# Performance work log

Hardware: AMD Instinct MI355X
Metric: run time of the kernel (lower is better)

Reference implementation:

```python
import jax, jax.numpy as jnp
import numpy as np

# --- constants from init_kwargs ---
ANCHORS = np.array([1.3221, 1.73145, 3.19275, 4.00944, 5.05587,
                    8.09892, 9.47112, 4.84053, 11.2364, 10.0071], np.float32).reshape(5, 2)
NA = 5           # num_anchors
NC = 1           # num_classes (per meta input)
CS = 20          # meta classes (target.size(1))
MAX_BOXES = 50
COORD_SCALE = 1.0
NOOBJ_SCALE = 1.0
OBJ_SCALE = 5.0
CLASS_SCALE = 1.0
SIL_THRESH = 0.6
N_META = 20      # enews buckets


def _iou(cx1, cy1, w1, h1, cx2, cy2, w2, h2):
    # center-format IoU, matching bbox_ious(..., x1y1x2y2=False)
    mx = jnp.minimum(cx1 - 0.5 * w1, cx2 - 0.5 * w2)
    Mx = jnp.maximum(cx1 + 0.5 * w1, cx2 + 0.5 * w2)
    my = jnp.minimum(cy1 - 0.5 * h1, cy2 - 0.5 * h2)
    My = jnp.maximum(cy1 + 0.5 * h1, cy2 + 0.5 * h2)
    cw = w1 + w2 - (Mx - mx)
    ch = h1 + h2 - (My - my)
    inter = jnp.where((cw > 0) & (ch > 0), cw * ch, 0.0)
    return inter / (w1 * h1 + w2 * h2 - inter)


def setup_inputs() -> dict:
    key = jax.random.key(0)
    k1, k2, k3, k4 = jax.random.split(key, 4)
    output = jax.random.normal(k1, (320, 30, 26, 26), dtype=jnp.float32)
    target = jax.random.uniform(k2, (16, 20, 250), dtype=jnp.float32)
    dynamic_weights = jax.random.normal(k3, (1, 64, 1024), dtype=jnp.float32)
    target_cls_ids = jax.random.randint(k4, (64,), 0, 20, dtype=jnp.int32)
    return {"output": output, "target": target,
            "dynamic_weights": dynamic_weights, "target_cls_ids": target_cls_ids}


def reference(output, target, dynamic_weights, target_cls_ids):
    target = jax.lax.stop_gradient(target)  # torch uses target.data
    dw = dynamic_weights[0]                 # (n_dw, D)

    nB, ch, nH, nW = output.shape
    bs = nB // CS
    K = NA * nH * nW
    out5 = output.reshape(nB, NA, 5 + NC, nH, nW)
    x = jax.nn.sigmoid(out5[:, :, 0])
    y = jax.nn.sigmoid(out5[:, :, 1])
    w = out5[:, :, 2]
    h = out5[:, :, 3]
    conf = jax.nn.sigmoid(out5[:, :, 4])
    # meta classification logits: softmax across the cs meta inputs
    cls_logits = out5[:, :, 5].reshape(bs, CS, K)  # nC == 1

    aw = jnp.asarray(ANCHORS[:, 0])
    ah = jnp.asarray(ANCHORS[:, 1])
    grid_x = jnp.arange(nW, dtype=jnp.float32)
    grid_y = jnp.arange(nH, dtype=jnp.float32)

    # decoded pred boxes (torch builds them from .data -> detached)
    px = jax.lax.stop_gradient(x) + grid_x[None, None, None, :]
    py = jax.lax.stop_gradient(y) + grid_y[None, None, :, None]
    pw = jnp.exp(jax.lax.stop_gradient(w)) * aw[None, :, None, None]
    ph = jnp.exp(jax.lax.stop_gradient(h)) * ah[None, :, None, None]

    # ---- build_targets (vectorized) ----
    g = target.reshape(nB, MAX_BOXES, 5)
    valid = g[:, :, 1] != 0
    gxs = g[:, :, 1] * nW
    gys = g[:, :, 2] * nH
    gws = g[:, :, 3] * nW
    ghs = g[:, :, 4] * nH

    pb = lambda t: t.reshape(nB, K, 1)
    ious = _iou(pb(px), pb(py), pb(pw), pb(ph),
                gxs[:, None, :], gys[:, None, :], gws[:, None, :], ghs[:, None, :])  # (nB,K,50)
    cur_ious = jnp.max(jnp.where(valid[:, None, :], ious, 0.0), axis=-1)
    conf_mask = jnp.where(cur_ious > SIL_THRESH, 0.0, NOOBJ_SCALE).reshape(nB, NA, nH, nW)

    # seen < 12800 branch (self.seen = 0)
    shape4 = (nB, NA, nH, nW)
    coord_mask = jnp.ones(shape4, jnp.float32)
    tx = jnp.full(shape4, 0.5, jnp.float32)
    ty = jnp.full(shape4, 0.5, jnp.float32)
    tw = jnp.zeros(shape4, jnp.float32)
    th = jnp.zeros(shape4, jnp.float32)
    tconf = jnp.zeros(shape4, jnp.float32)
    cls_mask = jnp.zeros(shape4, jnp.float32)

    # best anchor per gt by wh-IoU (anchor_step == 2)
    inter_a = jnp.minimum(gws[..., None], aw) * jnp.minimum(ghs[..., None], ah)
    iou_a = inter_a / (gws[..., None] * ghs[..., None] + aw * ah - inter_a)
    best_n = jnp.argmax(iou_a, axis=-1)  # (nB,50)

    gi = jnp.clip(gxs.astype(jnp.int32), 0, nW - 1)
    gj = jnp.clip(gys.astype(jnp.int32), 0, nH - 1)
    b_idx = jnp.broadcast_to(jnp.arange(nB)[:, None], (nB, MAX_BOXES))
    fidx = ((b_idx * NA + best_n) * nH + gj) * nW + gi
    fidx = jnp.where(valid, fidx, nB * NA * nH * nW).reshape(-1)  # OOB -> dropped

    def scat(base, vals):
        return base.reshape(-1).at[fidx].set(vals.reshape(-1), mode='drop').reshape(shape4)

    pbx = px[b_idx, best_n, gj, gi]
    pby = py[b_idx, best_n, gj, gi]
    pbw = pw[b_idx, best_n, gj, gi]
    pbh = ph[b_idx, best_n, gj, gi]
    iou_gt = _iou(gxs, gys, gws, ghs, pbx, pby, pbw, pbh)

    ones = jnp.ones_like(gxs)
    coord_mask = scat(coord_mask, ones)
    cls_mask = scat(cls_mask, ones)
    conf_mask = scat(conf_mask, jnp.full_like(gxs, OBJ_SCALE))
    tx = scat(tx, gxs - gi.astype(jnp.float32))
    ty = scat(ty, gys - gj.astype(jnp.float32))
    tw = scat(tw, jnp.log(gws / aw[best_n]))
    th = scat(th, jnp.log(ghs / ah[best_n]))
    tconf = scat(tconf, iou_gt)

    # ---- region losses ----
    loss_x = COORD_SCALE * 0.5 * jnp.sum(coord_mask * (x - tx) ** 2)
    loss_y = COORD_SCALE * 0.5 * jnp.sum(coord_mask * (y - ty) ** 2)
    loss_w = COORD_SCALE * 0.5 * jnp.sum(coord_mask * (w - tw) ** 2)
    loss_h = COORD_SCALE * 0.5 * jnp.sum(coord_mask * (h - th) ** 2)
    loss_conf = 0.5 * jnp.sum(conf_mask * (conf - tconf) ** 2)

    logp = jax.nn.log_softmax(jnp.transpose(cls_logits, (0, 2, 1)), axis=-1)  # (bs,K,CS)
    mask_bc = cls_mask.reshape(bs, CS, K)
    loss_cls = CLASS_SCALE * (-jnp.sum(mask_bc * jnp.transpose(logp, (0, 2, 1))))

    # ---- max-margin term over dynamic reweighting vectors ----
    cnt = jax.ops.segment_sum(jnp.ones(dw.shape[0], jnp.float32), target_cls_ids, N_META)
    sums = jax.ops.segment_sum(dw, target_cls_ids, N_META)
    enews = sums / jnp.maximum(cnt, 1.0)[:, None]
    present = cnt > 0
    same = jnp.sum((dw - enews[target_cls_ids]) ** 2)
    d = jnp.sum((enews[:, None, :] - enews[None, :, :]) ** 2, axis=-1)
    vp = present[:, None] & present[None, :] & (~jnp.eye(N_META, dtype=bool))
    dmin = jnp.min(jnp.where(vp, d, jnp.inf), axis=1)
    different = jnp.sum(jnp.where(jnp.any(vp, axis=1), dmin, 0.0))

    return loss_x + loss_y + loss_w + loss_h + loss_conf + loss_cls + same - different
```

## Files before the change

### kernel.cpp

```cpp
#include <hip/hip_runtime.h>
#include <math.h>

#define NB 320
#define NAC 5
#define NH 26
#define NW 26
#define CHW 676
#define KTOT 3380
#define BSTRIDE 20280
#define MAXB 50
#define CS 20
#define NMETA 20
#define DWROWS 64
#define DWDIM 1024
#define NPAIR (NMETA * NMETA)
#define NCBLK 4
#define NPARTR (NB * NCBLK)
#define NMETAY ((NSAMEPAIR + NCBLK - 1) / NCBLK)
#define NSAMEPAIR (NMETA + NPAIR)
#define NPART (NPARTR + NMETA)

__constant__ float c_aw[5] = {1.3221f, 3.19275f, 5.05587f, 9.47112f, 11.2364f};
__constant__ float c_ah[5] = {1.73145f, 4.00944f, 8.09892f, 4.84053f, 10.0071f};

__device__ __forceinline__ float rl_f(float v, int l) {
    return __int_as_float(__builtin_amdgcn_readlane(__float_as_int(v), l));
}

__global__ __launch_bounds__(256) void fused_k(const float* __restrict__ out,
                                               const float* __restrict__ target,
                                               const float* __restrict__ dw,
                                               const int* __restrict__ ids,
                                               float* __restrict__ part,
                                               float* __restrict__ dmat) {
    __shared__ float sred[4];
    int tid = threadIdx.x;
    int lane = tid & 63;
    int wid = tid >> 6;
    int b = blockIdx.y;

    if (b >= NB) {
        int p = (b - NB) * NCBLK + blockIdx.x;
        float s = 0.0f;
        if (p < NMETA) {
            int c = p;
            float acc[4] = {0, 0, 0, 0}, ssq[4] = {0, 0, 0, 0};
            int cnt = 0;
            for (int r = 0; r < DWROWS; r++) {
                int idr = ids[r];
                if (idr == c) {
                    cnt++;
#pragma unroll
                    for (int k = 0; k < 4; k++) {
                        float v = dw[r * DWDIM + tid + k * 256];
                        acc[k] += v; ssq[k] += v * v;
                    }
                }
            }
            if (cnt > 0) {
                float inv = 1.0f / (float)cnt;
#pragma unroll
                for (int k = 0; k < 4; k++) {
                    float e = acc[k] * inv;
                    s += ssq[k] - (float)cnt * e * e;
                }
            }
        } else {
            int pp = p - NMETA;
            int pi = pp / NMETA, pj = pp - pi * NMETA;
            if (pi != pj) {
                float ai[4] = {0, 0, 0, 0}, aj[4] = {0, 0, 0, 0};
                int ci = 0, cj = 0;
                for (int r = 0; r < DWROWS; r++) {
                    int idr = ids[r];
                    if (idr == pi) {
                        ci++;
#pragma unroll
                        for (int k = 0; k < 4; k++) ai[k] += dw[r * DWDIM + tid + k * 256];
                    } else if (idr == pj) {
                        cj++;
#pragma unroll
                        for (int k = 0; k < 4; k++) aj[k] += dw[r * DWDIM + tid + k * 256];
                    }
                }
                float ii = 1.0f / fmaxf((float)ci, 1.0f);
                float ij = 1.0f / fmaxf((float)cj, 1.0f);
#pragma unroll
                for (int k = 0; k < 4; k++) {
                    float df = ai[k] * ii - aj[k] * ij;
                    s += df * df;
                }
            }
        }
#pragma unroll
        for (int o = 32; o > 0; o >>= 1) s += __shfl_down(s, o, 64);
        if (lane == 0) sred[wid] = s;
        __syncthreads();
        if (tid == 0) {
            float tot = sred[0] + sred[1] + sred[2] + sred[3];
            if (p < NMETA) part[NPARTR + p] = tot;
            else dmat[p - NMETA] = tot;
        }
        return;
    }

    float blox = 1e30f, bhix = -1e30f, bloy = 1e30f, bhiy = -1e30f, bta = 0.0f;
    float gx = 0.0f, gy = 0.0f, gw = 0.0f, gh = 0.0f;
    bool bvalid;
    {
        int t = (lane < MAXB) ? lane : 0;
        const float* g = target + b * (MAXB * 5) + t * 5;
        float g1 = g[1];
        gx = g1 * (float)NW;
        gy = g[2] * (float)NH;
        gw = g[3] * (float)NW;
        gh = g[4] * (float)NH;
        bvalid = (g1 != 0.0f) && (lane < MAXB);
        if (bvalid) {
            blox = gx - 0.5f * gw; bhix = gx + 0.5f * gw;
            bloy = gy - 0.5f * gh; bhiy = gy + 0.5f * gh;
            bta = 0.375f * gw * gh;
        }
    }

    bool isbox = (blockIdx.x == NCBLK - 1) && (wid == 2);
    float contrib = 0.0f;

    if (!isbox) {
        int k0 = blockIdx.x * 1024 + tid * 4;
        if (k0 < KTOT) {
            int a = k0 / CHW;
            int rem0 = k0 - a * CHW;
            const float* base = out + (size_t)b * BSTRIDE + a * 6 * CHW + rem0;
            float4 R0 = *(const float4*)(base + 0 * CHW);
            float4 R1 = *(const float4*)(base + 1 * CHW);
            float4 R2 = *(const float4*)(base + 2 * CHW);
            float4 R3 = *(const float4*)(base + 3 * CHW);
            float4 R4 = *(const float4*)(base + 4 * CHW);
            float RX[4] = {R0.x, R0.y, R0.z, R0.w};
            float RY[4] = {R1.x, R1.y, R1.z, R1.w};
            float RW[4] = {R2.x, R2.y, R2.z, R2.w};
            float RH[4] = {R3.x, R3.y, R3.z, R3.w};
            float RC[4] = {R4.x, R4.y, R4.z, R4.w};
            float X[4], Y[4], CF[4];
            float PLOX[4], PHIX[4], PLOY[4], PHIY[4], THR[4], SM[4];
            float aw = c_aw[a], ah = c_ah[a];
#pragma unroll
            for (int c = 0; c < 4; c++) {
                int rem = rem0 + c;
                int i = rem / NW;
                int j = rem - i * NW;
                float x = 1.0f / (1.0f + __expf(-RX[c]));
                float y = 1.0f / (1.0f + __expf(-RY[c]));
                float conf = 1.0f / (1.0f + __expf(-RC[c]));
                float pw = __expf(RW[c]) * aw;
                float ph = __expf(RH[c]) * ah;
                float px = x + (float)j;
                float py = y + (float)i;
                PLOX[c] = px - 0.5f * pw; PHIX[c] = px + 0.5f * pw;
                PLOY[c] = py - 0.5f * ph; PHIY[c] = py + 0.5f * ph;
                THR[c] = 0.375f * (pw * ph);
                SM[c] = -1e30f;
                X[c] = x; Y[c] = y; CF[c] = conf;
            }
#pragma unroll 10
            for (int tb = 0; tb < MAXB; tb++) {
                float thix = rl_f(bhix, tb), tlox = rl_f(blox, tb);
                float thiy = rl_f(bhiy, tb), tloy = rl_f(bloy, tb);
                float ta   = rl_f(bta, tb);
#pragma unroll
                for (int c = 0; c < 4; c++) {
                    float ix = fminf(PHIX[c], thix) - fmaxf(PLOX[c], tlox);
                    float iy = fminf(PHIY[c], thiy) - fmaxf(PLOY[c], tloy);
                    float ixc = fmaxf(ix, 0.0f), iyc = fmaxf(iy, 0.0f);
                    SM[c] = fmaxf(SM[c], __builtin_fmaf(ixc, iyc, -ta));
                }
            }
#pragma unroll
            for (int c = 0; c < 4; c++) {
                float dx = X[c] - 0.5f, dy = Y[c] - 0.5f;
                contrib += 0.5f * (dx * dx + dy * dy + RW[c] * RW[c] + RH[c] * RH[c]);
                if (!(SM[c] > THR[c])) contrib += 0.5f * CF[c] * CF[c];
            }
        }
    } else {
        int t = lane;
        int fidx = -1 - t;
        int bn = 0, gi = 0, gj = 0;
        if (bvalid) {
            float area = gw * gh;
            float best = -1.0f;
#pragma unroll
            for (int n = 0; n < 5; n++) {
                float inter = fminf(gw, c_aw[n]) * fminf(gh, c_ah[n]);
                float iou = inter / (area + c_aw[n] * c_ah[n] - inter);
                if (iou > best) { best = iou; bn = n; }
            }
            gi = min(max((int)gx, 0), NW - 1);
            gj = min(max((int)gy, 0), NH - 1);
            fidx = (bn * NH + gj) * NW + gi;
        }
        bool winner = bvalid;
        for (int t2 = 1; t2 < MAXB; t2++) {
            int f2 = __builtin_amdgcn_readlane(fidx, t2);
            winner = winner && ((t2 <= t) || (f2 != fidx));
        }
        if (winner) {
            int rem = gj * NW + gi;
            const float* cell = out + (size_t)b * BSTRIDE + bn * 6 * CHW + rem;
            float rx = cell[0 * CHW];
            float ry = cell[1 * CHW];
            float w  = cell[2 * CHW];
            float h  = cell[3 * CHW];
            float rc = cell[4 * CHW];
            float x = 1.0f / (1.0f + __expf(-rx));
            float y = 1.0f / (1.0f + __expf(-ry));
            float conf = 1.0f / (1.0f + __expf(-rc));
            float aw = c_aw[bn], ah = c_ah[bn];
            float pw = __expf(w) * aw;
            float ph = __expf(h) * ah;
            float px = x + (float)gi;
            float py = y + (float)gj;
            float plox = px - 0.5f * pw, phix = px + 0.5f * pw;
            float ploy = py - 0.5f * ph, phiy = py + 0.5f * ph;
            float parea = pw * ph;
            float thr = 0.375f * parea;
            float smax = -1e30f;
            for (int tb = 0; tb < MAXB; tb++) {
                float thix = rl_f(bhix, tb), tlox = rl_f(blox, tb);
                float thiy = rl_f(bhiy, tb), tloy = rl_f(bloy, tb);
                float ta   = rl_f(bta, tb);
                float ix = fminf(phix, thix) - fmaxf(plox, tlox);
                float iy = fminf(phiy, thiy) - fmaxf(ploy, tloy);
                smax = fmaxf(smax, __builtin_fmaf(fmaxf(ix, 0.0f), fmaxf(iy, 0.0f), -ta));
            }
            bool silent = smax > thr;
            float dx0 = x - 0.5f, dy0 = y - 0.5f;
            float basel = 0.5f * (dx0 * dx0 + dy0 * dy0 + w * w + h * h);
            if (!silent) basel += 0.5f * conf * conf;
            float ix = fminf(phix, bhix) - fmaxf(plox, blox);
            float iy = fminf(phiy, bhiy) - fmaxf(ploy, bloy);
            float inter = fmaxf(ix, 0.0f) * fmaxf(iy, 0.0f);
            float iou = inter / (parea + gw * gh - inter);
            float txv = gx - (float)gi, tyv = gy - (float)gj;
            float twv = __logf(gw / aw), thv = __logf(gh / ah);
            float dx = x - txv, dy = y - tyv;
            float dwv = w - twv, dhv = h - thv;
            float dc = conf - iou;
            float ovr = 0.5f * (dx * dx + dy * dy + dwv * dwv + dhv * dhv) + 2.5f * dc * dc;
            int bs = b / CS, cs = b - bs * CS;
            const float* cl = out + (size_t)(bs * CS) * BSTRIDE + (bn * 6 + 5) * CHW + rem;
            float v[CS];
            float m = -1e30f;
#pragma unroll
            for (int c2 = 0; c2 < CS; c2++) { v[c2] = cl[(size_t)c2 * BSTRIDE]; m = fmaxf(m, v[c2]); }
            float s = 0.0f, own = 0.0f;
#pragma unroll
            for (int c2 = 0; c2 < CS; c2++) {
                s += __expf(v[c2] - m);
                if (c2 == cs) own = v[c2];
            }
            contrib = ovr - basel + (m + __logf(s)) - own;
        }
    }

#pragma unroll
    for (int o = 32; o > 0; o >>= 1) contrib += __shfl_down(contrib, o, 64);
    if (lane == 0) sred[wid] = contrib;
    __syncthreads();
    if (tid == 0) part[b * NCBLK + blockIdx.x] = sred[0] + sred[1] + sred[2] + sred[3];
}

__global__ __launch_bounds__(256) void finish_k(const int* __restrict__ ids,
                                                const float* __restrict__ part,
                                                const float* __restrict__ dmat,
                                                float* __restrict__ loss) {
    __shared__ float sred[4];
    __shared__ int scnt[NMETA];
    __shared__ float sdd;
    int tid = threadIdx.x;
    int lane = tid & 63, wid = tid >> 6;

    if (tid < NMETA) {
        int c = 0;
        for (int r = 0; r < DWROWS; r++) c += (ids[r] == tid) ? 1 : 0;
        scnt[tid] = c;
    }
    __syncthreads();
    float dd = 0.0f;
    if (tid < NMETA && scnt[tid] > 0) {
        float dmin = INFINITY;
        bool any = false;
        for (int j = 0; j < NMETA; j++) {
            if (j != tid && scnt[j] > 0) {
                any = true;
                dmin = fminf(dmin, dmat[tid * NMETA + j]);
            }
        }
        dd = any ? dmin : 0.0f;
    }
    if (tid < 64) {
#pragma unroll
        for (int o = 32; o > 0; o >>= 1) dd += __shfl_down(dd, o, 64);
        if (tid == 0) sdd = dd;
    }
    float ps = 0.0f;
    for (int i2 = tid; i2 < NPART; i2 += 256) ps += part[i2];
#pragma unroll
    for (int o = 32; o > 0; o >>= 1) ps += __shfl_down(ps, o, 64);
    if (lane == 0) sred[wid] = ps;
    __syncthreads();
    if (tid == 0) loss[0] = (sred[0] + sred[1] + sred[2] + sred[3]) - sdd;
}

extern "C" void kernel_launch(void* const* d_in, const int* in_sizes, int n_in,
                              void* d_out, int out_size, void* d_ws, size_t ws_size,
                              hipStream_t stream) {
    const float* output = (const float*)d_in[0];
    const float* target = (const float*)d_in[1];
    const float* dw     = (const float*)d_in[2];
    const int*   ids    = (const int*)d_in[3];
    float* loss = (float*)d_out;

    float* part = (float*)d_ws;
    float* dmat = part + NPART;

    dim3 grid(NCBLK, NB + NMETAY);
    fused_k<<<grid, 256, 0, stream>>>(output, target, dw, ids, part, dmat);
    finish_k<<<1, 256, 0, stream>>>(ids, part, dmat, loss);
}
```

Measured before the change: 104.4 us.

## Process eight cells per thread and stage GT boxes in shared memory

Each thread now handles eight anchor cells (two float4 groups) instead of four, which halves the number of column blocks per batch image. The ground-truth box bounds move from per-lane registers read with readlane into an LDS array broadcast to all waves, so each box costs one LDS read for eight cells. The box-handling wave shifts to wave 3, and the meta-pair blocks gain bounds guards to fit the new block count. It also drops the clamp on the y-overlap, which relies on the x-overlap clamp making the product non-positive. The trade-off is a longer per-thread serial loop and more register pressure, in exchange for fewer blocks and fewer redundant target loads.

```diff
diff --git a/kernel.cpp b/kernel.cpp
--- a/kernel.cpp
+++ b/kernel.cpp
@@ -14,10 +14,10 @@
 #define DWROWS 64
 #define DWDIM 1024
 #define NPAIR (NMETA * NMETA)
-#define NCBLK 4
+#define NCBLK 2
 #define NPARTR (NB * NCBLK)
+#define NSAMEPAIR (NMETA + NPAIR)
 #define NMETAY ((NSAMEPAIR + NCBLK - 1) / NCBLK)
-#define NSAMEPAIR (NMETA + NPAIR)
 #define NPART (NPARTR + NMETA)
 
 __constant__ float c_aw[5] = {1.3221f, 3.19275f, 5.05587f, 9.47112f, 11.2364f};
@@ -34,6 +34,8 @@
                                                float* __restrict__ part,
                                                float* __restrict__ dmat) {
     __shared__ float sred[4];
+    __shared__ float4 sbox[MAXB];
+    __shared__ float sta[MAXB];
     int tid = threadIdx.x;
     int lane = tid & 63;
     int wid = tid >> 6;
@@ -65,7 +67,7 @@
                     s += ssq[k] - (float)cnt * e * e;
                 }
             }
-        } else {
+        } else if (p < NSAMEPAIR) {
             int pp = p - NMETA;
             int pi = pp / NMETA, pj = pp - pi * NMETA;
             if (pi != pj) {
@@ -96,7 +98,7 @@
         for (int o = 32; o > 0; o >>= 1) s += __shfl_down(s, o, 64);
         if (lane == 0) sred[wid] = s;
         __syncthreads();
-        if (tid == 0) {
+        if (tid == 0 && p < NSAMEPAIR) {
             float tot = sred[0] + sred[1] + sred[2] + sred[3];
             if (p < NMETA) part[NPARTR + p] = tot;
             else dmat[p - NMETA] = tot;
@@ -104,87 +106,105 @@
         return;
     }
 
-    float blox = 1e30f, bhix = -1e30f, bloy = 1e30f, bhiy = -1e30f, bta = 0.0f;
-    float gx = 0.0f, gy = 0.0f, gw = 0.0f, gh = 0.0f;
-    bool bvalid;
-    {
-        int t = (lane < MAXB) ? lane : 0;
-        const float* g = target + b * (MAXB * 5) + t * 5;
+    if (tid < MAXB) {
+        const float* g = target + b * (MAXB * 5) + tid * 5;
         float g1 = g[1];
-        gx = g1 * (float)NW;
-        gy = g[2] * (float)NH;
-        gw = g[3] * (float)NW;
-        gh = g[4] * (float)NH;
-        bvalid = (g1 != 0.0f) && (lane < MAXB);
-        if (bvalid) {
-            blox = gx - 0.5f * gw; bhix = gx + 0.5f * gw;
-            bloy = gy - 0.5f * gh; bhiy = gy + 0.5f * gh;
-            bta = 0.375f * gw * gh;
-        }
-    }
-
-    bool isbox = (blockIdx.x == NCBLK - 1) && (wid == 2);
+        float gx = g1 * (float)NW;
+        float gy = g[2] * (float)NH;
+        float gw = g[3] * (float)NW;
+        float gh = g[4] * (float)NH;
+        float4 e;
+        float ta;
+        if (g1 != 0.0f) {
+            e.x = gx - 0.5f * gw; e.y = gx + 0.5f * gw;
+            e.z = gy - 0.5f * gh; e.w = gy + 0.5f * gh;
+            ta = 0.375f * gw * gh;
+        } else {
+            e.x = 1e30f; e.y = -1e30f; e.z = 1e30f; e.w = -1e30f;
+            ta = 0.0f;
+        }
+        sbox[tid] = e;
+        sta[tid] = ta;
+    }
+    __syncthreads();
+
+    bool isbox = (blockIdx.x == NCBLK - 1) && (wid == 3);
     float contrib = 0.0f;
 
     if (!isbox) {
-        int k0 = blockIdx.x * 1024 + tid * 4;
-        if (k0 < KTOT) {
-            int a = k0 / CHW;
-            int rem0 = k0 - a * CHW;
-            const float* base = out + (size_t)b * BSTRIDE + a * 6 * CHW + rem0;
-            float4 R0 = *(const float4*)(base + 0 * CHW);
-            float4 R1 = *(const float4*)(base + 1 * CHW);
-            float4 R2 = *(const float4*)(base + 2 * CHW);
-            float4 R3 = *(const float4*)(base + 3 * CHW);
-            float4 R4 = *(const float4*)(base + 4 * CHW);
-            float RX[4] = {R0.x, R0.y, R0.z, R0.w};
-            float RY[4] = {R1.x, R1.y, R1.z, R1.w};
-            float RW[4] = {R2.x, R2.y, R2.z, R2.w};
-            float RH[4] = {R3.x, R3.y, R3.z, R3.w};
-            float RC[4] = {R4.x, R4.y, R4.z, R4.w};
-            float X[4], Y[4], CF[4];
-            float PLOX[4], PHIX[4], PLOY[4], PHIY[4], THR[4], SM[4];
-            float aw = c_aw[a], ah = c_ah[a];
-#pragma unroll
-            for (int c = 0; c < 4; c++) {
-                int rem = rem0 + c;
-                int i = rem / NW;
-                int j = rem - i * NW;
-                float x = 1.0f / (1.0f + __expf(-RX[c]));
-                float y = 1.0f / (1.0f + __expf(-RY[c]));
-                float conf = 1.0f / (1.0f + __expf(-RC[c]));
-                float pw = __expf(RW[c]) * aw;
-                float ph = __expf(RH[c]) * ah;
-                float px = x + (float)j;
-                float py = y + (float)i;
-                PLOX[c] = px - 0.5f * pw; PHIX[c] = px + 0.5f * pw;
-                PLOY[c] = py - 0.5f * ph; PHIY[c] = py + 0.5f * ph;
-                THR[c] = 0.375f * (pw * ph);
-                SM[c] = -1e30f;
-                X[c] = x; Y[c] = y; CF[c] = conf;
-            }
-#pragma unroll 10
+        int k0 = blockIdx.x * 2048 + tid * 8;
+        float PLOX[8], PHIX[8], PLOY[8], PHIY[8], THR[8], CF[8], SM[8];
+        int ng = 0;
+#pragma unroll
+        for (int g4 = 0; g4 < 2; g4++) {
+            int kg = k0 + g4 * 4;
+            if (kg < KTOT) {
+                int a = kg / CHW;
+                int rem0 = kg - a * CHW;
+                const float* base = out + (size_t)b * BSTRIDE + a * 6 * CHW + rem0;
+                float4 R0 = *(const float4*)(base + 0 * CHW);
+                float4 R1 = *(const float4*)(base + 1 * CHW);
+                float4 R2 = *(const float4*)(base + 2 * CHW);
+                float4 R3 = *(const float4*)(base + 3 * CHW);
+                float4 R4 = *(const float4*)(base + 4 * CHW);
+                float RX[4] = {R0.x, R0.y, R0.z, R0.w};
+                float RY[4] = {R1.x, R1.y, R1.z, R1.w};
+                float RW[4] = {R2.x, R2.y, R2.z, R2.w};
+                float RH[4] = {R3.x, R3.y, R3.z, R3.w};
+                float RC[4] = {R4.x, R4.y, R4.z, R4.w};
+                float aw = c_aw[a], ah = c_ah[a];
+#pragma unroll
+                for (int c = 0; c < 4; c++) {
+                    int rem = rem0 + c;
+                    int i = rem / NW;
+                    int j = rem - i * NW;
+                    float x = 1.0f / (1.0f + __expf(-RX[c]));
+                    float y = 1.0f / (1.0f + __expf(-RY[c]));
+                    float conf = 1.0f / (1.0f + __expf(-RC[c]));
+                    float pw = __expf(RW[c]) * aw;
+                    float ph = __expf(RH[c]) * ah;
+                    float px = x + (float)j;
+                    float py = y + (float)i;
+                    int q = ng + c;
+                    PLOX[q] = px - 0.5f * pw; PHIX[q] = px + 0.5f * pw;
+                    PLOY[q] = py - 0.5f * ph; PHIY[q] = py + 0.5f * ph;
+                    THR[q] = 0.375f * (pw * ph);
+                    SM[q] = -1e30f;
+                    CF[q] = conf;
+                    float dx = x - 0.5f, dy = y - 0.5f;
+                    contrib += 0.5f * (dx * dx + dy * dy + RW[c] * RW[c] + RH[c] * RH[c]);
+                }
+                ng += 4;
+            }
+        }
+        if (ng > 0) {
             for (int tb = 0; tb < MAXB; tb++) {
-                float thix = rl_f(bhix, tb), tlox = rl_f(blox, tb);
-                float thiy = rl_f(bhiy, tb), tloy = rl_f(bloy, tb);
-                float ta   = rl_f(bta, tb);
-#pragma unroll
-                for (int c = 0; c < 4; c++) {
-                    float ix = fminf(PHIX[c], thix) - fmaxf(PLOX[c], tlox);
-                    float iy = fminf(PHIY[c], thiy) - fmaxf(PLOY[c], tloy);
-                    float ixc = fmaxf(ix, 0.0f), iyc = fmaxf(iy, 0.0f);
-                    SM[c] = fmaxf(SM[c], __builtin_fmaf(ixc, iyc, -ta));
-                }
-            }
-#pragma unroll
-            for (int c = 0; c < 4; c++) {
-                float dx = X[c] - 0.5f, dy = Y[c] - 0.5f;
-                contrib += 0.5f * (dx * dx + dy * dy + RW[c] * RW[c] + RH[c] * RH[c]);
-                if (!(SM[c] > THR[c])) contrib += 0.5f * CF[c] * CF[c];
+                float4 e = sbox[tb];
+                float ta = sta[tb];
+#pragma unroll
+                for (int q = 0; q < 8; q++) {
+                    if (q >= ng) break;
+                    float ix = fminf(PHIX[q], e.y) - fmaxf(PLOX[q], e.x);
+                    float iy = fminf(PHIY[q], e.w) - fmaxf(PLOY[q], e.z);
+                    SM[q] = fmaxf(SM[q], __builtin_fmaf(fmaxf(ix, 0.0f), iy, -ta));
+                }
+            }
+#pragma unroll
+            for (int q = 0; q < 8; q++) {
+                if (q >= ng) break;
+                if (!(SM[q] > THR[q])) contrib += 0.5f * CF[q] * CF[q];
             }
         }
     } else {
         int t = lane;
+        const float* g = target + b * (MAXB * 5) + ((t < MAXB) ? t : 0) * 5;
+        float g1 = g[1];
+        float gx = g1 * (float)NW;
+        float gy = g[2] * (float)NH;
+        float gw = g[3] * (float)NW;
+        float gh = g[4] * (float)NH;
+        bool bvalid = (g1 != 0.0f) && (t < MAXB);
+
         int fidx = -1 - t;
         int bn = 0, gi = 0, gj = 0;
         if (bvalid) {
@@ -227,17 +247,18 @@
             float thr = 0.375f * parea;
             float smax = -1e30f;
             for (int tb = 0; tb < MAXB; tb++) {
-                float thix = rl_f(bhix, tb), tlox = rl_f(blox, tb);
-                float thiy = rl_f(bhiy, tb), tloy = rl_f(bloy, tb);
-                float ta   = rl_f(bta, tb);
-                float ix = fminf(phix, thix) - fmaxf(plox, tlox);
-                float iy = fminf(phiy, thiy) - fmaxf(ploy, tloy);
-                smax = fmaxf(smax, __builtin_fmaf(fmaxf(ix, 0.0f), fmaxf(iy, 0.0f), -ta));
+                float4 e = sbox[tb];
+                float ta = sta[tb];
+                float ix = fminf(phix, e.y) - fmaxf(plox, e.x);
+                float iy = fminf(phiy, e.w) - fmaxf(ploy, e.z);
+                smax = fmaxf(smax, __builtin_fmaf(fmaxf(ix, 0.0f), iy, -ta));
             }
             bool silent = smax > thr;
             float dx0 = x - 0.5f, dy0 = y - 0.5f;
             float basel = 0.5f * (dx0 * dx0 + dy0 * dy0 + w * w + h * h);
             if (!silent) basel += 0.5f * conf * conf;
+            float blox = gx - 0.5f * gw, bhix = gx + 0.5f * gw;
+            float bloy = gy - 0.5f * gh, bhiy = gy + 0.5f * gh;
             float ix = fminf(phix, bhix) - fmaxf(plox, blox);
             float iy = fminf(phiy, bhiy) - fmaxf(ploy, bloy);
             float inter = fmaxf(ix, 0.0f) * fmaxf(iy, 0.0f);
```

After: 109.4 us. +4.8%, slower.
